# Kernel tuning notes

Measured on AMD Instinct MI355X. Metric: run time of the kernel, lower is better.

The kernel has to match this reference:

```python
import jax, jax.numpy as jnp
import numpy as np

COMMITMENT = 0.25
EPS = 1e-12  # F.normalize default eps


def _l2norm(x, axis=-1):
    n = jnp.sqrt(jnp.sum(x * x, axis=axis, keepdims=True))
    return x / jnp.maximum(n, EPS)


def _wn(g, v):
    # torch weight_norm(Linear) with dim=0: per-output-row normalization
    return g[:, None] * v / jnp.maximum(jnp.sqrt(jnp.sum(v * v, axis=1, keepdims=True)), EPS)


def setup_inputs() -> dict:
    key = jax.random.key(0)
    ks = jax.random.split(key, 8)
    B, D, T = 16, 1024, 4096
    CS, CD = 1024, 8
    return {
        "z": jax.random.normal(ks[0], (B, D, T), dtype=jnp.float32),
        "codebook": jax.random.normal(ks[1], (CS, CD), dtype=jnp.float32),
        "g_in": jax.random.uniform(ks[2], (CD,), dtype=jnp.float32) + 0.5,
        "v_in": jax.random.normal(ks[3], (CD, D), dtype=jnp.float32) * 0.02,
        "b_in": jax.random.normal(ks[4], (CD,), dtype=jnp.float32) * 0.02,
        "g_out": jax.random.uniform(ks[5], (D,), dtype=jnp.float32) + 0.5,
        "v_out": jax.random.normal(ks[6], (D, CD), dtype=jnp.float32) * 0.02,
        "b_out": jax.random.normal(ks[7], (D,), dtype=jnp.float32) * 0.02,
    }


def reference(z, codebook, g_in, v_in, b_in, g_out, v_out, b_out):
    B, D, T = z.shape
    CS, CD = codebook.shape
    W_in = _wn(g_in, v_in)    # [CD, D]
    W_out = _wn(g_out, v_out)  # [D, CD]

    # in_proj: (b t d) @ W_in^T + b -> expressed directly on [B, D, T]
    z_e = jnp.einsum("bdt,cd->bct", z, W_in) + b_in[None, :, None]  # [B, CD, T]

    # decode_latents: cosine-distance nearest neighbor over codebook
    enc = z_e.transpose(0, 2, 1).reshape(B * T, CD)
    enc_n = _l2norm(enc)
    cb_n = _l2norm(codebook)
    dist = (
        jnp.sum(enc_n * enc_n, axis=1, keepdims=True)
        - 2.0 * enc_n @ cb_n.T
        + jnp.sum(cb_n * cb_n, axis=1)[None, :]
    )  # [B*T, CS]
    indices = jnp.argmax(-dist, axis=1).reshape(B, T)  # [B, T]

    # gather from the UN-normalized codebook (embed_code uses raw weights)
    z_q = codebook[indices].transpose(0, 2, 1)  # [B, CD, T]

    sg = jax.lax.stop_gradient
    commitment_loss = jnp.mean((z_e - sg(z_q)) ** 2, axis=(1, 2)) * COMMITMENT
    codebook_loss = jnp.mean((z_q - sg(z_e)) ** 2, axis=(1, 2))
    commit_loss = commitment_loss + codebook_loss  # [B]

    # straight-through estimator
    z_q_st = z_e + sg(z_q - z_e)  # [B, CD, T]

    out = jnp.einsum("bct,dc->bdt", z_q_st, W_out) + b_out[None, :, None]  # [B, D, T]
    return out, indices, commit_loss
```

## Files before the change

kernel.cpp:

```cpp
#include <hip/hip_runtime.h>
#include <math.h>
#include <stdint.h>

#define B_ 16
#define D_ 1024
#define T_ 4096
#define CS_ 1024
#define CD_ 8

__device__ __forceinline__ float f_tree8(const float r[8]) {
  return __fadd_rn(
      __fadd_rn(__fadd_rn(r[0], r[1]), __fadd_rn(r[2], r[3])),
      __fadd_rn(__fadd_rn(r[4], r[5]), __fadd_rn(r[6], r[7])));
}
__device__ __forceinline__ float f_sumsq8(const float x[8]) {
  float s[8];
#pragma unroll
  for (int k = 0; k < 8; ++k) s[k] = __fmul_rn(x[k], x[k]);
  return f_tree8(s);
}

__global__ __launch_bounds__(1024) void vq_setup(
    const float* __restrict__ cb, const float* __restrict__ g_in,
    const float* __restrict__ v_in, const float* __restrict__ g_out,
    const float* __restrict__ v_out, const float* __restrict__ b_out,
    double* __restrict__ WTd, float* __restrict__ cb16,
    float* __restrict__ wo16) {
  __shared__ float sv[8 * 1024];
  __shared__ float leafs[64];
  __shared__ float den[8];
  const int tid = threadIdx.x;

  for (int i = tid; i < 8 * 1024; i += 1024) sv[i] = v_in[i];
  __syncthreads();

  if (tid < 64) {
    const int c = tid >> 3, l = tid & 7;
    const float* a = sv + c * 1024 + l * 128;
    float r[8];
#pragma unroll
    for (int k = 0; k < 8; ++k) r[k] = __fmul_rn(a[k], a[k]);
    for (int i = 8; i < 128; i += 8) {
#pragma unroll
      for (int k = 0; k < 8; ++k)
        r[k] = __fadd_rn(r[k], __fmul_rn(a[i + k], a[i + k]));
    }
    leafs[c * 8 + l] = f_tree8(r);
  }
  __syncthreads();
  if (tid < 8) {
    const float* L = leafs + tid * 8;
    float lr[8];
#pragma unroll
    for (int k = 0; k < 8; ++k) lr[k] = L[k];
    const float s = f_tree8(lr);
    den[tid] = fmaxf(__fsqrt_rn(s), 1e-12f);
  }
  __syncthreads();

  if (tid < 1024) {
#pragma unroll
    for (int c = 0; c < 8; ++c) {
      const float w = __fdiv_rn(__fmul_rn(g_in[c], sv[c * 1024 + tid]), den[c]);
      WTd[tid * 8 + c] = (double)w;
    }
    {
      const float* cr = cb + tid * 8;
      float q[8];
#pragma unroll
      for (int c = 0; c < 8; ++c) q[c] = cr[c];
      const float nn = f_sumsq8(q);
      const float dd = fmaxf(__fsqrt_rn(nn), 1e-12f);
      float qn[8];
#pragma unroll
      for (int c = 0; c < 8; ++c) {
        qn[c] = __fdiv_rn(q[c], dd);
        cb16[tid * 16 + c] = qn[c];
      }
      cb16[tid * 16 + 8] = f_sumsq8(qn);
#pragma unroll
      for (int c = 9; c < 16; ++c) cb16[tid * 16 + c] = 0.f;
    }
    {
      const float* vr = v_out + tid * 8;
      float w[8];
#pragma unroll
      for (int c = 0; c < 8; ++c) w[c] = vr[c];
      const float n2 = f_sumsq8(w);
      const float d2 = fmaxf(__fsqrt_rn(n2), 1e-12f);
      const float go = g_out[tid];
#pragma unroll
      for (int c = 0; c < 8; ++c)
        wo16[tid * 16 + c] = __fdiv_rn(__fmul_rn(go, w[c]), d2);
      wo16[tid * 16 + 8] = b_out[tid];
#pragma unroll
      for (int c = 9; c < 16; ++c) wo16[tid * 16 + c] = 0.f;
    }
  }
}

__global__ __launch_bounds__(1024, 8) void vq_main(
    const float* __restrict__ z, const float* __restrict__ cbraw,
    const float* __restrict__ b_in, const double* __restrict__ WTd,
    const float* __restrict__ cb16, const float* __restrict__ wo16,
    float* __restrict__ out, float* __restrict__ oidx,
    float* __restrict__ lossp) {
  __shared__ double accb[8192];
  const int tid = threadIdx.x;
  const int q0 = __builtin_amdgcn_readfirstlane(tid >> 6);
  const int tl = tid & 63;
  const int blk = blockIdx.x;
  const int b = blk >> 5;
  const int tile = blk & 31;
  const int t0 = tile * 128 + tl * 2;

  const float2* zp2 =
      (const float2*)(z + ((size_t)b * D_ + (size_t)q0 * 64) * T_ + t0);
  const double* wd = WTd + (size_t)q0 * 512;

  double acc0[8], acc1[8];
#pragma unroll
  for (int c = 0; c < 8; ++c) { acc0[c] = 0.0; acc1[c] = 0.0; }

  float2 zA[8], zB[8];
#pragma unroll
  for (int u = 0; u < 8; ++u) zA[u] = zp2[(size_t)u * (T_ / 2)];

#pragma unroll
  for (int dc = 0; dc < 64; dc += 16) {
#pragma unroll
    for (int u = 0; u < 8; ++u)
      zB[u] = zp2[(size_t)(dc + 8 + u) * (T_ / 2)];
#pragma unroll
    for (int u = 0; u < 8; ++u) {
      const double* w = wd + (size_t)(dc + u) * 8;
      const double zx = (double)zA[u].x, zy = (double)zA[u].y;
#pragma unroll
      for (int c = 0; c < 8; ++c) {
        acc0[c] = fma(zx, w[c], acc0[c]);
        acc1[c] = fma(zy, w[c], acc1[c]);
      }
    }
    if (dc + 16 < 64) {
#pragma unroll
      for (int u = 0; u < 8; ++u)
        zA[u] = zp2[(size_t)(dc + 16 + u) * (T_ / 2)];
    }
#pragma unroll
    for (int u = 0; u < 8; ++u) {
      const double* w = wd + (size_t)(dc + 8 + u) * 8;
      const double zx = (double)zB[u].x, zy = (double)zB[u].y;
#pragma unroll
      for (int c = 0; c < 8; ++c) {
        acc0[c] = fma(zx, w[c], acc0[c]);
        acc1[c] = fma(zy, w[c], acc1[c]);
      }
    }
  }

  double2* accb2 = (double2*)accb;
  double tot0[8], tot1[8];
#pragma unroll
  for (int half = 0; half < 2; ++half) {
    const int cb0 = half * 4;
#pragma unroll
    for (int c = 0; c < 4; ++c) {
      double2 v; v.x = acc0[cb0 + c]; v.y = acc1[cb0 + c];
      accb2[c * 1024 + tid] = v;
    }
    __syncthreads();
#pragma unroll
    for (int c = 0; c < 4; ++c) {
      const double2* row = accb2 + c * 1024 + tl;
      double2 s = row[0];
#pragma unroll
      for (int qq = 1; qq < 16; ++qq) {
        const double2 v = row[qq * 64];
        s.x = s.x + v.x;
        s.y = s.y + v.y;
      }
      tot0[cb0 + c] = s.x; tot1[cb0 + c] = s.y;
    }
    __syncthreads();
  }

  float e0[8], e1[8], en0[8], en1[8];
#pragma unroll
  for (int c = 0; c < 8; ++c) {
    e0[c] = __fadd_rn((float)tot0[c], b_in[c]);
    e1[c] = __fadd_rn((float)tot1[c], b_in[c]);
  }
  const float n20 = f_sumsq8(e0), n21 = f_sumsq8(e1);
  const float dn0 = fmaxf(__fsqrt_rn(n20), 1e-12f);
  const float dn1 = fmaxf(__fsqrt_rn(n21), 1e-12f);
#pragma unroll
  for (int c = 0; c < 8; ++c) {
    en0[c] = __fdiv_rn(e0[c], dn0);
    en1[c] = __fdiv_rn(e1[c], dn1);
  }
  const float s_enc0 = f_sumsq8(en0), s_enc1 = f_sumsq8(en1);

  const int j0 = q0 * 64;
  float best0 = INFINITY, best1 = INFINITY;
  int bj0 = j0, bj1 = j0;
  {
    const float* cbq = cb16 + (size_t)j0 * 16;
#pragma unroll 4
    for (int jj = 0; jj < 64; ++jj) {
      const float* row = cbq + jj * 16;
      const float4 lo = *(const float4*)(row);
      const float4 hi = *(const float4*)(row + 4);
      const float sc = row[8];
      float d0 = 0.f, d1 = 0.f;
      d0 = fmaf(en0[0], lo.x, d0); d1 = fmaf(en1[0], lo.x, d1);
      d0 = fmaf(en0[1], lo.y, d0); d1 = fmaf(en1[1], lo.y, d1);
      d0 = fmaf(en0[2], lo.z, d0); d1 = fmaf(en1[2], lo.z, d1);
      d0 = fmaf(en0[3], lo.w, d0); d1 = fmaf(en1[3], lo.w, d1);
      d0 = fmaf(en0[4], hi.x, d0); d1 = fmaf(en1[4], hi.x, d1);
      d0 = fmaf(en0[5], hi.y, d0); d1 = fmaf(en1[5], hi.y, d1);
      d0 = fmaf(en0[6], hi.z, d0); d1 = fmaf(en1[6], hi.z, d1);
      d0 = fmaf(en0[7], hi.w, d0); d1 = fmaf(en1[7], hi.w, d1);
      const float dist0 =
          __fadd_rn(__fsub_rn(s_enc0, __fmul_rn(2.0f, d0)), sc);
      const float dist1 =
          __fadd_rn(__fsub_rn(s_enc1, __fmul_rn(2.0f, d1)), sc);
      if (dist0 < best0) { best0 = dist0; bj0 = j0 + jj; }
      if (dist1 < best1) { best1 = dist1; bj1 = j0 + jj; }
    }
  }

  float* distf0 = (float*)accb;
  int* candj0 = (int*)((char*)accb + 4096);
  float* distf1 = (float*)((char*)accb + 8192);
  int* candj1 = (int*)((char*)accb + 12288);
  distf0[tid] = best0; candj0[tid] = bj0;
  distf1[tid] = best1; candj1[tid] = bj1;
  __syncthreads();

  float bd0 = distf0[tl], bd1 = distf1[tl];
  int bi0 = candj0[tl], bi1 = candj1[tl];
#pragma unroll
  for (int qq = 1; qq < 16; ++qq) {
    const float dd0 = distf0[qq * 64 + tl];
    const int jj0v = candj0[qq * 64 + tl];
    if (dd0 < bd0) { bd0 = dd0; bi0 = jj0v; }
    const float dd1 = distf1[qq * 64 + tl];
    const int jj1v = candj1[qq * 64 + tl];
    if (dd1 < bd1) { bd1 = dd1; bi1 = jj1v; }
  }

  if (tid < 64) {
    float2 iv; iv.x = (float)bi0; iv.y = (float)bi1;
    *(float2*)(oidx + (size_t)b * T_ + t0) = iv;
  }

  float cq0[8], cq1[8];
  {
    const float* cp0 = cbraw + (size_t)bi0 * 8;
    const float* cp1 = cbraw + (size_t)bi1 * 8;
#pragma unroll
    for (int c = 0; c < 8; ++c) { cq0[c] = cp0[c]; cq1[c] = cp1[c]; }
  }

  if (tid < 64) {
    float lsum = 0.f;
#pragma unroll
    for (int c = 0; c < 8; ++c) {
      const float df0 = __fsub_rn(e0[c], cq0[c]);
      lsum = fmaf(df0, df0, lsum);
    }
#pragma unroll
    for (int c = 0; c < 8; ++c) {
      const float df1 = __fsub_rn(e1[c], cq1[c]);
      lsum = fmaf(df1, df1, lsum);
    }
#pragma unroll
    for (int off = 32; off > 0; off >>= 1)
      lsum += __shfl_down(lsum, off, 64);
    if (tl == 0) lossp[blk] = lsum;
  }

  float2* op2 =
      (float2*)(out + ((size_t)b * D_ + (size_t)q0 * 64) * T_ + t0);
  const float* woq = wo16 + (size_t)q0 * 1024;
#pragma unroll 4
  for (int d = 0; d < 64; ++d) {
    const float* row = woq + d * 16;
    const float4 lo = *(const float4*)(row);
    const float4 hi = *(const float4*)(row + 4);
    const float bo = row[8];
    float d0 = 0.f, d1 = 0.f;
    d0 = fmaf(cq0[0], lo.x, d0); d1 = fmaf(cq1[0], lo.x, d1);
    d0 = fmaf(cq0[1], lo.y, d0); d1 = fmaf(cq1[1], lo.y, d1);
    d0 = fmaf(cq0[2], lo.z, d0); d1 = fmaf(cq1[2], lo.z, d1);
    d0 = fmaf(cq0[3], lo.w, d0); d1 = fmaf(cq1[3], lo.w, d1);
    d0 = fmaf(cq0[4], hi.x, d0); d1 = fmaf(cq1[4], hi.x, d1);
    d0 = fmaf(cq0[5], hi.y, d0); d1 = fmaf(cq1[5], hi.y, d1);
    d0 = fmaf(cq0[6], hi.z, d0); d1 = fmaf(cq1[6], hi.z, d1);
    d0 = fmaf(cq0[7], hi.w, d0); d1 = fmaf(cq1[7], hi.w, d1);
    float2 ov; ov.x = __fadd_rn(d0, bo); ov.y = __fadd_rn(d1, bo);
    op2[(size_t)d * (T_ / 2)] = ov;
  }
}

__global__ __launch_bounds__(64) void vq_fin(const float* __restrict__ lossp,
                                             float* __restrict__ oloss) {
  const int tid = threadIdx.x;
  if (tid < B_) {
    float s = 0.f;
    for (int i = 0; i < 32; ++i) s += lossp[tid * 32 + i];
    oloss[tid] = s * (1.25f / 32768.0f);
  }
}

extern "C" void kernel_launch(void* const* d_in, const int* in_sizes, int n_in,
                              void* d_out, int out_size, void* d_ws,
                              size_t ws_size, hipStream_t stream) {
  (void)in_sizes; (void)n_in; (void)out_size; (void)ws_size;
  const float* z = (const float*)d_in[0];
  const float* cb = (const float*)d_in[1];
  const float* g_in = (const float*)d_in[2];
  const float* v_in = (const float*)d_in[3];
  const float* b_in = (const float*)d_in[4];
  const float* g_out = (const float*)d_in[5];
  const float* v_out = (const float*)d_in[6];
  const float* b_out = (const float*)d_in[7];
  float* out = (float*)d_out;

  char* ws = (char*)d_ws;
  double* WTd = (double*)ws;
  float* cb16 = (float*)(ws + 65536);
  float* wo16 = (float*)(ws + 131072);
  float* lossp = (float*)(ws + 196608);

  float* oidx = out + (size_t)B_ * D_ * T_;
  float* oloss = oidx + (size_t)B_ * T_;

  vq_setup<<<1, 1024, 0, stream>>>(cb, g_in, v_in, g_out, v_out, b_out, WTd,
                                   cb16, wo16);
  vq_main<<<512, 1024, 0, stream>>>(z, cb, b_in, WTd, cb16, wo16, out, oidx,
                                    lossp);
  vq_fin<<<1, 64, 0, stream>>>(lossp, oloss);
}
```

Baseline: 151.0 us.

## Reduce cross-wave reductions in one wave, broadcast via LDS; shrink z prefetch

The cross-wave reductions of the projection accumulators and of the argmin candidates are now done by the first wave only, with results published through shared memory and broadcast after an extra barrier. Before, all 16 waves repeated the same reduction. The z double-buffer also shrinks from 8 to 4 rows per stage, with sched_barrier fences added to pin load/compute ordering. This cuts redundant LDS reads and VGPR pressure but adds barriers and serialises the reduction onto one wave.

```diff
diff --git a/kernel.cpp b/kernel.cpp
--- a/kernel.cpp
+++ b/kernel.cpp
@@ -105,7 +105,7 @@
     const float* __restrict__ cb16, const float* __restrict__ wo16,
     float* __restrict__ out, float* __restrict__ oidx,
     float* __restrict__ lossp) {
-  __shared__ double accb[8192];
+  __shared__ double accb[8704];
   const int tid = threadIdx.x;
   const int q0 = __builtin_amdgcn_readfirstlane(tid >> 6);
   const int tl = tid & 63;
@@ -122,17 +122,18 @@
 #pragma unroll
   for (int c = 0; c < 8; ++c) { acc0[c] = 0.0; acc1[c] = 0.0; }
 
-  float2 zA[8], zB[8];
-#pragma unroll
-  for (int u = 0; u < 8; ++u) zA[u] = zp2[(size_t)u * (T_ / 2)];
-
-#pragma unroll
-  for (int dc = 0; dc < 64; dc += 16) {
-#pragma unroll
-    for (int u = 0; u < 8; ++u)
-      zB[u] = zp2[(size_t)(dc + 8 + u) * (T_ / 2)];
-#pragma unroll
-    for (int u = 0; u < 8; ++u) {
+  float2 zA[4], zB[4];
+#pragma unroll
+  for (int u = 0; u < 4; ++u) zA[u] = zp2[(size_t)u * (T_ / 2)];
+
+#pragma unroll
+  for (int dc = 0; dc < 64; dc += 8) {
+#pragma unroll
+    for (int u = 0; u < 4; ++u)
+      zB[u] = zp2[(size_t)(dc + 4 + u) * (T_ / 2)];
+    __builtin_amdgcn_sched_barrier(0);
+#pragma unroll
+    for (int u = 0; u < 4; ++u) {
       const double* w = wd + (size_t)(dc + u) * 8;
       const double zx = (double)zA[u].x, zy = (double)zA[u].y;
 #pragma unroll
@@ -141,14 +142,15 @@
         acc1[c] = fma(zy, w[c], acc1[c]);
       }
     }
-    if (dc + 16 < 64) {
-#pragma unroll
-      for (int u = 0; u < 8; ++u)
-        zA[u] = zp2[(size_t)(dc + 16 + u) * (T_ / 2)];
-    }
-#pragma unroll
-    for (int u = 0; u < 8; ++u) {
-      const double* w = wd + (size_t)(dc + 8 + u) * 8;
+    if (dc + 8 < 64) {
+#pragma unroll
+      for (int u = 0; u < 4; ++u)
+        zA[u] = zp2[(size_t)(dc + 8 + u) * (T_ / 2)];
+    }
+    __builtin_amdgcn_sched_barrier(0);
+#pragma unroll
+    for (int u = 0; u < 4; ++u) {
+      const double* w = wd + (size_t)(dc + 4 + u) * 8;
       const double zx = (double)zB[u].x, zy = (double)zB[u].y;
 #pragma unroll
       for (int c = 0; c < 8; ++c) {
@@ -159,29 +161,37 @@
   }
 
   double2* accb2 = (double2*)accb;
+  double2* totb = accb2 + 4096;
   double tot0[8], tot1[8];
 #pragma unroll
   for (int half = 0; half < 2; ++half) {
-    const int cb0 = half * 4;
+    const int c0 = half * 4;
 #pragma unroll
     for (int c = 0; c < 4; ++c) {
-      double2 v; v.x = acc0[cb0 + c]; v.y = acc1[cb0 + c];
+      double2 v; v.x = acc0[c0 + c]; v.y = acc1[c0 + c];
       accb2[c * 1024 + tid] = v;
     }
     __syncthreads();
+    if (tid < 64) {
+#pragma unroll
+      for (int c = 0; c < 4; ++c) {
+        const double2* row = accb2 + c * 1024 + tl;
+        double2 s = row[0];
+#pragma unroll
+        for (int qq = 1; qq < 16; ++qq) {
+          const double2 v = row[qq * 64];
+          s.x = s.x + v.x;
+          s.y = s.y + v.y;
+        }
+        totb[c * 64 + tl] = s;
+      }
+    }
+    __syncthreads();
 #pragma unroll
     for (int c = 0; c < 4; ++c) {
-      const double2* row = accb2 + c * 1024 + tl;
-      double2 s = row[0];
-#pragma unroll
-      for (int qq = 1; qq < 16; ++qq) {
-        const double2 v = row[qq * 64];
-        s.x = s.x + v.x;
-        s.y = s.y + v.y;
-      }
-      tot0[cb0 + c] = s.x; tot1[cb0 + c] = s.y;
-    }
-    __syncthreads();
+      const double2 s = totb[c * 64 + tl];
+      tot0[c0 + c] = s.x; tot1[c0 + c] = s.y;
+    }
   }
 
   float e0[8], e1[8], en0[8], en1[8];
@@ -233,26 +243,30 @@
   int* candj0 = (int*)((char*)accb + 4096);
   float* distf1 = (float*)((char*)accb + 8192);
   int* candj1 = (int*)((char*)accb + 12288);
+  int* ibuf = (int*)((char*)accb + 16384);
   distf0[tid] = best0; candj0[tid] = bj0;
   distf1[tid] = best1; candj1[tid] = bj1;
   __syncthreads();
 
-  float bd0 = distf0[tl], bd1 = distf1[tl];
-  int bi0 = candj0[tl], bi1 = candj1[tl];
-#pragma unroll
-  for (int qq = 1; qq < 16; ++qq) {
-    const float dd0 = distf0[qq * 64 + tl];
-    const int jj0v = candj0[qq * 64 + tl];
-    if (dd0 < bd0) { bd0 = dd0; bi0 = jj0v; }
-    const float dd1 = distf1[qq * 64 + tl];
-    const int jj1v = candj1[qq * 64 + tl];
-    if (dd1 < bd1) { bd1 = dd1; bi1 = jj1v; }
-  }
-
   if (tid < 64) {
-    float2 iv; iv.x = (float)bi0; iv.y = (float)bi1;
+    float bd0 = distf0[tl], bd1 = distf1[tl];
+    int ci0 = candj0[tl], ci1 = candj1[tl];
+#pragma unroll
+    for (int qq = 1; qq < 16; ++qq) {
+      float dd = distf0[qq * 64 + tl];
+      int jj = candj0[qq * 64 + tl];
+      if (dd < bd0) { bd0 = dd; ci0 = jj; }
+      dd = distf1[qq * 64 + tl];
+      jj = candj1[qq * 64 + tl];
+      if (dd < bd1) { bd1 = dd; ci1 = jj; }
+    }
+    ibuf[tl] = ci0; ibuf[64 + tl] = ci1;
+    float2 iv; iv.x = (float)ci0; iv.y = (float)ci1;
     *(float2*)(oidx + (size_t)b * T_ + t0) = iv;
   }
+  __syncthreads();
+  const int bi0 = ibuf[tid & 63];
+  const int bi1 = ibuf[64 + (tid & 63)];
 
   float cq0[8], cq1[8];
   {
```

After: 158.8 us. +5.2%, slower.

## Split fused VQ kernel into encode/argmin and separate output projection kernels

Applied to the files above, without the earlier changes.

The single main kernel is split into vq_ze, which computes z_e, the codebook argmin, the indices and the loss partials, and a new vq_out kernel that reads the indices back and writes the 256 MB output with float4 stores, four timesteps per thread. The cross-wave reduction of z_e is now done once by the first wave and broadcast through shared memory, and the argmin, gather and loss work is limited to that wave. The intent is to decouple the write-heavy output stage from the read-heavy, occupancy-limited encode stage and to widen its stores. In exchange it adds a kernel launch and a round trip of the indices through global memory, and vq_ze now skips the codebook gather for the other 15 waves.

```diff
diff --git a/kernel.cpp b/kernel.cpp
--- a/kernel.cpp
+++ b/kernel.cpp
@@ -99,13 +99,12 @@
   }
 }
 
-__global__ __launch_bounds__(1024, 8) void vq_main(
+__global__ __launch_bounds__(1024, 8) void vq_ze(
     const float* __restrict__ z, const float* __restrict__ cbraw,
     const float* __restrict__ b_in, const double* __restrict__ WTd,
-    const float* __restrict__ cb16, const float* __restrict__ wo16,
-    float* __restrict__ out, float* __restrict__ oidx,
+    const float* __restrict__ cb16, float* __restrict__ oidx,
     float* __restrict__ lossp) {
-  __shared__ double accb[8192];
+  __shared__ double accb[8704];
   const int tid = threadIdx.x;
   const int q0 = __builtin_amdgcn_readfirstlane(tid >> 6);
   const int tl = tid & 63;
@@ -159,29 +158,37 @@
   }
 
   double2* accb2 = (double2*)accb;
+  double2* totb = accb2 + 4096;
   double tot0[8], tot1[8];
 #pragma unroll
   for (int half = 0; half < 2; ++half) {
-    const int cb0 = half * 4;
+    const int c0 = half * 4;
 #pragma unroll
     for (int c = 0; c < 4; ++c) {
-      double2 v; v.x = acc0[cb0 + c]; v.y = acc1[cb0 + c];
+      double2 v; v.x = acc0[c0 + c]; v.y = acc1[c0 + c];
       accb2[c * 1024 + tid] = v;
     }
     __syncthreads();
+    if (tid < 64) {
+#pragma unroll
+      for (int c = 0; c < 4; ++c) {
+        const double2* row = accb2 + c * 1024 + tl;
+        double2 s = row[0];
+#pragma unroll
+        for (int qq = 1; qq < 16; ++qq) {
+          const double2 v = row[qq * 64];
+          s.x = s.x + v.x;
+          s.y = s.y + v.y;
+        }
+        totb[c * 64 + tl] = s;
+      }
+    }
+    __syncthreads();
 #pragma unroll
     for (int c = 0; c < 4; ++c) {
-      const double2* row = accb2 + c * 1024 + tl;
-      double2 s = row[0];
-#pragma unroll
-      for (int qq = 1; qq < 16; ++qq) {
-        const double2 v = row[qq * 64];
-        s.x = s.x + v.x;
-        s.y = s.y + v.y;
-      }
-      tot0[cb0 + c] = s.x; tot1[cb0 + c] = s.y;
-    }
-    __syncthreads();
+      const double2 s = totb[c * 64 + tl];
+      tot0[c0 + c] = s.x; tot1[c0 + c] = s.y;
+    }
   }
 
   float e0[8], e1[8], en0[8], en1[8];
@@ -237,32 +244,26 @@
   distf1[tid] = best1; candj1[tid] = bj1;
   __syncthreads();
 
-  float bd0 = distf0[tl], bd1 = distf1[tl];
-  int bi0 = candj0[tl], bi1 = candj1[tl];
-#pragma unroll
-  for (int qq = 1; qq < 16; ++qq) {
-    const float dd0 = distf0[qq * 64 + tl];
-    const int jj0v = candj0[qq * 64 + tl];
-    if (dd0 < bd0) { bd0 = dd0; bi0 = jj0v; }
-    const float dd1 = distf1[qq * 64 + tl];
-    const int jj1v = candj1[qq * 64 + tl];
-    if (dd1 < bd1) { bd1 = dd1; bi1 = jj1v; }
-  }
-
   if (tid < 64) {
+    float bd0 = distf0[tl], bd1 = distf1[tl];
+    int bi0 = candj0[tl], bi1 = candj1[tl];
+#pragma unroll
+    for (int qq = 1; qq < 16; ++qq) {
+      float dd = distf0[qq * 64 + tl];
+      int jj = candj0[qq * 64 + tl];
+      if (dd < bd0) { bd0 = dd; bi0 = jj; }
+      dd = distf1[qq * 64 + tl];
+      jj = candj1[qq * 64 + tl];
+      if (dd < bd1) { bd1 = dd; bi1 = jj; }
+    }
     float2 iv; iv.x = (float)bi0; iv.y = (float)bi1;
     *(float2*)(oidx + (size_t)b * T_ + t0) = iv;
-  }
-
-  float cq0[8], cq1[8];
-  {
+
+    float cq0[8], cq1[8];
     const float* cp0 = cbraw + (size_t)bi0 * 8;
     const float* cp1 = cbraw + (size_t)bi1 * 8;
 #pragma unroll
     for (int c = 0; c < 8; ++c) { cq0[c] = cp0[c]; cq1[c] = cp1[c]; }
-  }
-
-  if (tid < 64) {
     float lsum = 0.f;
 #pragma unroll
     for (int c = 0; c < 8; ++c) {
@@ -279,27 +280,63 @@
       lsum += __shfl_down(lsum, off, 64);
     if (tl == 0) lossp[blk] = lsum;
   }
-
-  float2* op2 =
-      (float2*)(out + ((size_t)b * D_ + (size_t)q0 * 64) * T_ + t0);
-  const float* woq = wo16 + (size_t)q0 * 1024;
+}
+
+__global__ __launch_bounds__(256) void vq_out(
+    const float* __restrict__ cbraw, const float* __restrict__ wo16,
+    const float* __restrict__ oidx, float* __restrict__ out) {
+  const int tid = threadIdx.x;
+  const int blk = blockIdx.x;
+  const int b = blk >> 6;
+  const int tq = (blk >> 4) & 3;
+  const int dq = blk & 15;
+  const int t0 = tq * 1024 + tid * 4;
+  const int d0 = dq * 64;
+
+  const float4 iv = *(const float4*)(oidx + (size_t)b * T_ + t0);
+  const int i0 = (int)iv.x, i1 = (int)iv.y, i2 = (int)iv.z, i3 = (int)iv.w;
+
+  float cq0[8], cq1[8], cq2[8], cq3[8];
+  {
+    const float* p0 = cbraw + (size_t)i0 * 8;
+    const float* p1 = cbraw + (size_t)i1 * 8;
+    const float* p2 = cbraw + (size_t)i2 * 8;
+    const float* p3 = cbraw + (size_t)i3 * 8;
+#pragma unroll
+    for (int c = 0; c < 8; ++c) {
+      cq0[c] = p0[c]; cq1[c] = p1[c]; cq2[c] = p2[c]; cq3[c] = p3[c];
+    }
+  }
+
+  const float* woq = wo16 + (size_t)d0 * 16;
+  float* op = out + ((size_t)b * D_ + d0) * T_ + t0;
 #pragma unroll 4
   for (int d = 0; d < 64; ++d) {
     const float* row = woq + d * 16;
     const float4 lo = *(const float4*)(row);
     const float4 hi = *(const float4*)(row + 4);
     const float bo = row[8];
-    float d0 = 0.f, d1 = 0.f;
-    d0 = fmaf(cq0[0], lo.x, d0); d1 = fmaf(cq1[0], lo.x, d1);
-    d0 = fmaf(cq0[1], lo.y, d0); d1 = fmaf(cq1[1], lo.y, d1);
-    d0 = fmaf(cq0[2], lo.z, d0); d1 = fmaf(cq1[2], lo.z, d1);
-    d0 = fmaf(cq0[3], lo.w, d0); d1 = fmaf(cq1[3], lo.w, d1);
-    d0 = fmaf(cq0[4], hi.x, d0); d1 = fmaf(cq1[4], hi.x, d1);
-    d0 = fmaf(cq0[5], hi.y, d0); d1 = fmaf(cq1[5], hi.y, d1);
-    d0 = fmaf(cq0[6], hi.z, d0); d1 = fmaf(cq1[6], hi.z, d1);
-    d0 = fmaf(cq0[7], hi.w, d0); d1 = fmaf(cq1[7], hi.w, d1);
-    float2 ov; ov.x = __fadd_rn(d0, bo); ov.y = __fadd_rn(d1, bo);
-    op2[(size_t)d * (T_ / 2)] = ov;
+    float o0 = 0.f, o1 = 0.f, o2 = 0.f, o3 = 0.f;
+    o0 = fmaf(cq0[0], lo.x, o0); o1 = fmaf(cq1[0], lo.x, o1);
+    o2 = fmaf(cq2[0], lo.x, o2); o3 = fmaf(cq3[0], lo.x, o3);
+    o0 = fmaf(cq0[1], lo.y, o0); o1 = fmaf(cq1[1], lo.y, o1);
+    o2 = fmaf(cq2[1], lo.y, o2); o3 = fmaf(cq3[1], lo.y, o3);
+    o0 = fmaf(cq0[2], lo.z, o0); o1 = fmaf(cq1[2], lo.z, o1);
+    o2 = fmaf(cq2[2], lo.z, o2); o3 = fmaf(cq3[2], lo.z, o3);
+    o0 = fmaf(cq0[3], lo.w, o0); o1 = fmaf(cq1[3], lo.w, o1);
+    o2 = fmaf(cq2[3], lo.w, o2); o3 = fmaf(cq3[3], lo.w, o3);
+    o0 = fmaf(cq0[4], hi.x, o0); o1 = fmaf(cq1[4], hi.x, o1);
+    o2 = fmaf(cq2[4], hi.x, o2); o3 = fmaf(cq3[4], hi.x, o3);
+    o0 = fmaf(cq0[5], hi.y, o0); o1 = fmaf(cq1[5], hi.y, o1);
+    o2 = fmaf(cq2[5], hi.y, o2); o3 = fmaf(cq3[5], hi.y, o3);
+    o0 = fmaf(cq0[6], hi.z, o0); o1 = fmaf(cq1[6], hi.z, o1);
+    o2 = fmaf(cq2[6], hi.z, o2); o3 = fmaf(cq3[6], hi.z, o3);
+    o0 = fmaf(cq0[7], hi.w, o0); o1 = fmaf(cq1[7], hi.w, o1);
+    o2 = fmaf(cq2[7], hi.w, o2); o3 = fmaf(cq3[7], hi.w, o3);
+    float4 ov;
+    ov.x = __fadd_rn(o0, bo); ov.y = __fadd_rn(o1, bo);
+    ov.z = __fadd_rn(o2, bo); ov.w = __fadd_rn(o3, bo);
+    *(float4*)(op + (size_t)d * T_) = ov;
   }
 }
 
@@ -338,7 +375,7 @@
 
   vq_setup<<<1, 1024, 0, stream>>>(cb, g_in, v_in, g_out, v_out, b_out, WTd,
                                    cb16, wo16);
-  vq_main<<<512, 1024, 0, stream>>>(z, cb, b_in, WTd, cb16, wo16, out, oidx,
-                                    lossp);
+  vq_ze<<<512, 1024, 0, stream>>>(z, cb, b_in, WTd, cb16, oidx, lossp);
+  vq_out<<<1024, 256, 0, stream>>>(cb, wo16, oidx, out);
   vq_fin<<<1, 64, 0, stream>>>(lossp, oloss);
 }
```

Result: slower. 197.1 us (+30.5%).
